# Kernel optimization log

Measured on AMD Instinct MI355X. Metric: run time of the kernel, lower is better.

## Reference

```python
import jax, jax.numpy as jnp
import numpy as np

B, L, DIM, N, D = 8, 273, 1536, 12, 128
ZS, F_HIS = 256, 32  # image tokens per frame, cache_frame_max
EPS = 1e-6


def rmsnorm(x, g, eps=EPS):
    return x * jax.lax.rsqrt(jnp.mean(x * x, axis=-1, keepdims=True) + eps) * g


def rope_apply(x, freqs):
    # x: [B, T, N, D]; freqs: [T, D//2] angles. Rotate consecutive pairs.
    xp = x.reshape(*x.shape[:-1], D // 2, 2)
    c = jnp.cos(freqs)[None, :, None, :]
    s = jnp.sin(freqs)[None, :, None, :]
    o1 = xp[..., 0] * c - xp[..., 1] * s
    o2 = xp[..., 0] * s + xp[..., 1] * c
    return jnp.stack([o1, o2], axis=-1).reshape(x.shape)


def setup_inputs() -> dict:
    key = jax.random.key(0)
    ks = jax.random.split(key, 10)
    rn = lambda k, shp, sc=1.0: jax.random.normal(k, shp, dtype=jnp.float32) * sc
    return {
        "x": rn(ks[0], (B, L, DIM)),
        "w_q": rn(ks[1], (DIM, DIM), 0.02), "b_q": jnp.zeros((DIM,), jnp.float32),
        "w_k": rn(ks[2], (DIM, DIM), 0.02), "b_k": jnp.zeros((DIM,), jnp.float32),
        "w_v": rn(ks[3], (DIM, DIM), 0.02), "b_v": jnp.zeros((DIM,), jnp.float32),
        "w_o": rn(ks[4], (DIM, DIM), 0.02), "b_o": jnp.zeros((DIM,), jnp.float32),
        "g_q": jnp.ones((DIM,), jnp.float32), "g_k": jnp.ones((DIM,), jnp.float32),
        "cache_k": rn(ks[5], (B, F_HIS * L, N, D)),
        "cache_v": rn(ks[6], (B, F_HIS * L, N, D)),
        "rope_table": jax.random.uniform(ks[7], (64, L, D // 2), dtype=jnp.float32) * (2.0 * np.pi),
        "read_rope_indices": jnp.arange(F_HIS, dtype=jnp.int32),
        "current_frame_idx": 20,
    }


def reference(x, w_q, b_q, w_k, b_k, w_v, b_v, w_o, b_o, g_q, g_k,
              cache_k, cache_v, rope_table, read_rope_indices, current_frame_idx):
    b, s = x.shape[:2]
    f = 1  # one new frame per step (s == L)
    # qkv projections with RMSNorm over full dim (pre head split)
    q = rmsnorm(x @ w_q.T + b_q, g_q).reshape(b, s, N, D)
    k = rmsnorm(x @ w_k.T + b_k, g_k).reshape(b, s, N, D)
    v = (x @ w_v.T + b_v).reshape(b, s, N, D)
    # KV-cache ring-buffer store at slot = frame_idx % cache_frame_max
    slot = current_frame_idx % F_HIS
    cache_k = jax.lax.dynamic_update_slice(cache_k, k, (0, slot * L, 0, 0))
    cache_v = jax.lax.dynamic_update_slice(cache_v, v, (0, slot * L, 0, 0))
    # RoPE angles: history for each cache slot, last for the current frame
    freqs_his = rope_table[read_rope_indices].reshape(F_HIS * L, D // 2)
    freqs_last = rope_table[current_frame_idx]  # [L, D//2]
    q_r = rope_apply(q, freqs_last)
    k_r = rope_apply(cache_k, freqs_his)
    # frame-major views: [b, frames, tokens_per_frame, n, d]
    q_r = q_r.reshape(b, f, L, N, D)
    k_r = k_r.reshape(b, F_HIS, L, N, D)
    v_his = cache_v.reshape(b, F_HIS, L, N, D)
    q_img, k_img, v_img = q_r[:, :, :ZS], k_r[:, :, :ZS], v_his[:, :, :ZS]
    # temporal attention per spatial (image) token, non-causal, masked to valid frames
    scale = 1.0 / jnp.sqrt(jnp.asarray(D, jnp.float32))
    scores = jnp.einsum('bfznd,bgznd->bznfg', q_img, k_img) * scale  # [b,zs,n,f,f_his]
    valid = jnp.minimum(current_frame_idx + 1, F_HIS)
    keep = jnp.arange(F_HIS) < valid
    scores = jnp.where(keep[None, None, None, None, :], scores, -1e30)
    p = jax.nn.softmax(scores, axis=-1)
    x_img = jnp.einsum('bznfg,bgznd->bfznd', p, v_img)  # [b, f, zs, n, d]
    # condition tokens bypass attention: pass through v of the current frame
    v_cond = v.reshape(b, f, L, N, D)[:, :, ZS:]
    out = jnp.concatenate([x_img, v_cond], axis=2).reshape(b, s, N * D)
    return out @ w_o.T + b_o


if __name__ == '__main__':
    o = reference(**setup_inputs())
    print(o.shape)
```

## Files before the change

kernel.cpp:

```cpp
#include <hip/hip_runtime.h>
#include <hip/hip_bf16.h>
#include <stdint.h>

typedef unsigned short u16;
typedef __attribute__((ext_vector_type(8))) short bf16x8;
typedef __attribute__((ext_vector_type(4))) float f32x4;

#define B_    8
#define L_    273
#define DIM_  1536
#define NH_   12
#define DH_   128
#define ZS_   256
#define FH_   32
#define MROWS (B_ * L_)
#define MPAD  2304
#define NQKV  4608
#define WN_   (DIM_ * DIM_)
#define WN8_  (WN_ / 8)
#define X8_   (MROWS * DIM_ / 8)
#define XT8_  (MPAD * DIM_ / 8)

#define N0_ 442368
#define N1_ 737280
#define N2_ 1032192
#define N3_ 1327104
#define N4_ 1622016
#define N5_ 1626624
#define N6_ 2167296
#define PREP_BLKS 8466

#define ATTN_ITEMS (B_ * ZS_ * 6)
#define ATTN_BLKS  (ATTN_ITEMS / 2)
#define VCOND_TOT  (B_ * (L_ - ZS_) * DIM_ / 8)
#define VCOND_BLKS ((VCOND_TOT + 255) / 256)

#define KSPLIT 768

#define OFF_XB    0ULL
#define OFF_WB    7077888ULL
#define OFF_WOB   21233664ULL
#define OFF_BQKV  25952256ULL
#define OFF_CQKV  25970688ULL
#define OFF_ATTN  47204352ULL
#define OFF_SC    54282240ULL
#define OFF_RMS   58607616ULL
#define OFF_P0    0ULL
#define OFF_P1    25970688ULL

__device__ __forceinline__ u16 f2bf(float f) {
  __hip_bfloat16 h = __float2bfloat16(f);
  return *reinterpret_cast<u16*>(&h);
}
__device__ __forceinline__ float bf2f(u16 v) {
  uint32_t u = ((uint32_t)v) << 16;
  return __uint_as_float(u);
}

__device__ __forceinline__ void gload_lds16(const u16* g, u16* l) {
  __builtin_amdgcn_global_load_lds(
      (const __attribute__((address_space(1))) void*)g,
      (__attribute__((address_space(3))) void*)l,
      16, 0, 0);
}

__device__ __forceinline__ void cast8(const float* __restrict__ s, u16* __restrict__ d,
                                      int i, int nvalid) {
  uint4 o;
  if (i < nvalid) {
    const float4 a = ((const float4*)s)[i * 2];
    const float4 b = ((const float4*)s)[i * 2 + 1];
    o.x = (uint32_t)f2bf(a.x) | ((uint32_t)f2bf(a.y) << 16);
    o.y = (uint32_t)f2bf(a.z) | ((uint32_t)f2bf(a.w) << 16);
    o.z = (uint32_t)f2bf(b.x) | ((uint32_t)f2bf(b.y) << 16);
    o.w = (uint32_t)f2bf(b.z) | ((uint32_t)f2bf(b.w) << 16);
  } else {
    o = make_uint4(0, 0, 0, 0);
  }
  ((uint4*)d)[i] = o;
}

__global__ __launch_bounds__(256)
void prep_kernel(const float* __restrict__ x, const float* __restrict__ w_q,
                 const float* __restrict__ w_k, const float* __restrict__ w_v,
                 const float* __restrict__ w_o, const float* __restrict__ bq,
                 const float* __restrict__ bk, const float* __restrict__ bv,
                 const float* __restrict__ rope_tb, const int* __restrict__ rope_ix,
                 const int* __restrict__ cf_ptr,
                 u16* __restrict__ xb, u16* __restrict__ wb, u16* __restrict__ wob,
                 float* __restrict__ bqkv, float* __restrict__ sctab) {
  const int t = blockIdx.x * 256 + threadIdx.x;
  if (t < N0_)      cast8(x,   xb,           t,       X8_);
  else if (t < N1_) cast8(w_q, wb,           t - N0_, WN8_);
  else if (t < N2_) cast8(w_k, wb + WN_,     t - N1_, WN8_);
  else if (t < N3_) cast8(w_v, wb + 2 * WN_, t - N2_, WN8_);
  else if (t < N4_) cast8(w_o, wob,          t - N3_, WN8_);
  else if (t < N5_) {
    int i = t - N4_;
    float v;
    if (i < DIM_)          v = bq[i];
    else if (i < 2 * DIM_) v = bk[i - DIM_];
    else                   v = bv[i - 2 * DIM_];
    bqkv[i] = v;
  } else if (t < N6_) {
    int u = t - N5_;
    int j = u & 63;
    int idx = u >> 6;
    int f = idx >> 8, z = idx & 255;
    int fi = (f == 32) ? *cf_ptr : rope_ix[f];
    float fr = rope_tb[((size_t)fi * L_ + z) * 64 + j];
    float sn, cn;
    __sincosf(fr, &sn, &cn);
    *(float2*)&sctab[((size_t)idx << 7) + 2 * j] = make_float2(sn, cn);
  }
}

__global__ __launch_bounds__(256)
void gemm_bt_kernel(const u16* __restrict__ A, const u16* __restrict__ Bm,
                    const float* __restrict__ bias, void* __restrict__ Cv,
                    void* __restrict__ Cv2,
                    int K, int ldc, int Mvalid, int mode, int ksplit) {
  const int nwg = gridDim.x * gridDim.y;
  const int lin = blockIdx.y * gridDim.x + blockIdx.x;
  const int nl = (lin & 7) * (nwg >> 3) + (lin >> 3);
  const int tn = nl % gridDim.x, tm = nl / gridDim.x;

  const int tid = threadIdx.x;
  const int lane = tid & 63;
  const int wid = tid >> 6;
  const int wm = wid >> 1, wn = wid & 1;

  __shared__ __align__(16) u16 As[2][128 * 32];
  __shared__ __align__(16) u16 Bs[2][128 * 32];

  f32x4 acc[4][4] = {};

  const int srow = tid >> 2;
  const int scol = (tid & 3) * 8;
  const u16* Abase = A + (size_t)(tm * 128 + srow) * K + scol;
  const u16* Bbase = Bm + (size_t)(tn * 128 + srow) * K + scol;
  const size_t rstep = (size_t)64 * K;
  const int lofs = srow * 32 + scol;

  const int ko = (lane >> 4) * 8;
  const int rA = wm * 64 + (lane & 15);
  const int rB = wn * 64 + (lane & 15);

  const int k0 = blockIdx.z * ksplit;
  const int k1 = k0 + ksplit;

  gload_lds16(Abase + k0,         &As[0][lofs]);
  gload_lds16(Abase + k0 + rstep, &As[0][64 * 32 + lofs]);
  gload_lds16(Bbase + k0,         &Bs[0][lofs]);
  gload_lds16(Bbase + k0 + rstep, &Bs[0][64 * 32 + lofs]);
  __syncthreads();

  int cur = 0;
  for (int kt = k0; kt < k1; kt += 32) {
    const int nx = cur ^ 1;
    if (kt + 32 < k1) {
      gload_lds16(Abase + kt + 32,         &As[nx][lofs]);
      gload_lds16(Abase + kt + 32 + rstep, &As[nx][64 * 32 + lofs]);
      gload_lds16(Bbase + kt + 32,         &Bs[nx][lofs]);
      gload_lds16(Bbase + kt + 32 + rstep, &Bs[nx][64 * 32 + lofs]);
    }
    bf16x8 af[4], bfr[4];
#pragma unroll
    for (int f = 0; f < 4; ++f) {
      af[f]  = *(const bf16x8*)&As[cur][(rA + f * 16) * 32 + ko];
      bfr[f] = *(const bf16x8*)&Bs[cur][(rB + f * 16) * 32 + ko];
    }
#pragma unroll
    for (int fm = 0; fm < 4; ++fm)
#pragma unroll
      for (int fn = 0; fn < 4; ++fn)
        acc[fm][fn] = __builtin_amdgcn_mfma_f32_16x16x32_bf16(af[fm], bfr[fn], acc[fm][fn], 0, 0, 0);
    __syncthreads();
    cur = nx;
  }

  const int m0 = tm * 128 + wm * 64 + (lane >> 4) * 4;
  const int n0 = tn * 128 + wn * 64 + (lane & 15);
  float* Cf = (mode == 2 && blockIdx.z) ? (float*)Cv2 : (float*)Cv;
#pragma unroll
  for (int fm = 0; fm < 4; ++fm) {
#pragma unroll
    for (int fn = 0; fn < 4; ++fn) {
      const int n = n0 + fn * 16;
      const float bv = (mode == 2) ? 0.f : bias[n];
#pragma unroll
      for (int r = 0; r < 4; ++r) {
        const int m = m0 + fm * 16 + r;
        if (m < Mvalid) {
          const float val = acc[fm][fn][r] + bv;
          if (mode == 1) ((u16*)Cv)[(size_t)m * ldc + n] = f2bf(val);
          else           Cf[(size_t)m * ldc + n] = val;
        }
      }
    }
  }
}

__global__ __launch_bounds__(256)
void rms_kernel(const u16* __restrict__ Cq, float* __restrict__ rms) {
  const int w = blockIdx.x * 4 + (threadIdx.x >> 6);
  const int lane = threadIdx.x & 63;
  const int sec = w & 1;
  const int rid = w >> 1;
  const int b = rid >> 8, z = rid & 255;
  const u16* p = Cq + (size_t)(b * L_ + z) * NQKV + sec * DIM_;
  float ss = 0.f;
#pragma unroll
  for (int j = 0; j < 3; ++j) {
    bf16x8 v = *(const bf16x8*)&p[lane * 8 + j * 512];
#pragma unroll
    for (int e = 0; e < 8; ++e) {
      float f = bf2f((u16)v[e]);
      ss += f * f;
    }
  }
#pragma unroll
  for (int o = 32; o; o >>= 1) ss += __shfl_xor(ss, o);
  if (lane == 0)
    rms[sec * 2048 + rid] = rsqrtf(ss * (1.f / DIM_) + 1e-6f);
}

__global__ __launch_bounds__(256)
void attention_kernel(const u16* __restrict__ Cq, const float* __restrict__ cache_k,
                      const float* __restrict__ cache_v, const float* __restrict__ sctab,
                      const float* __restrict__ rms, const float* __restrict__ g_q,
                      const float* __restrict__ g_k,
                      const int* __restrict__ cf_ptr, u16* __restrict__ attn_in) {
  if (blockIdx.x >= ATTN_BLKS) {
    int i = (blockIdx.x - ATTN_BLKS) * 256 + threadIdx.x;
    if (i < VCOND_TOT) {
      int e = i * 8;
      int col = e % DIM_;
      int r = e / DIM_;
      int b = r / (L_ - ZS_);
      int lz = r % (L_ - ZS_);
      size_t mrow = (size_t)b * L_ + ZS_ + lz;
      *(uint4*)&attn_in[mrow * DIM_ + col] = *(const uint4*)&Cq[mrow * NQKV + 2 * DIM_ + col];
    }
    return;
  }

  __shared__ float sm[2][64][6];
  const int p = threadIdx.x >> 7;
  const int wi = (threadIdx.x >> 6) & 1;
  const int lane = threadIdx.x & 63;
  const int item = blockIdx.x * 2 + p;
  const int hp = item % 6;
  const int z = (item / 6) % ZS_;
  const int b = item / (6 * ZS_);
  const int h = lane >> 5, il = lane & 31;
  const int n = hp * 2 + h;
  const int d0 = il * 4;
  const int cf = *cf_ptr;
  const int slot = cf % FH_;
  const int valid = min(cf + 1, FH_);
  const int g0 = (valid + 1) >> 1;
  const int gs = wi ? g0 : 0;
  const int ge = wi ? valid : g0;

  const size_t crow = (size_t)(b * L_ + z) * NQKV + n * DH_ + d0;
  const float rq = rms[b * ZS_ + z];
  float q0, q1, q2, q3;
  {
    ushort4 qv = *(const ushort4*)&Cq[crow];
    const float4 gq = *(const float4*)&g_q[n * DH_ + d0];
    const float u0 = bf2f(qv.x) * rq * gq.x;
    const float u1 = bf2f(qv.y) * rq * gq.y;
    const float u2 = bf2f(qv.z) * rq * gq.z;
    const float u3 = bf2f(qv.w) * rq * gq.w;
    const float4 scq = *(const float4*)&sctab[((size_t)(32 * ZS_ + z) << 7) + d0];
    q0 = u0 * scq.y - u1 * scq.x;
    q1 = u0 * scq.x + u1 * scq.y;
    q2 = u2 * scq.w - u3 * scq.z;
    q3 = u2 * scq.z + u3 * scq.w;
  }

  float mx = -1e30f, lsum = 0.f;
  float a0 = 0.f, a1 = 0.f, a2 = 0.f, a3 = 0.f;
  for (int g = gs; g < ge; ++g) {
    const float4 sc = *(const float4*)&sctab[((size_t)(g * ZS_ + z) << 7) + d0];
    float k0, k1, k2, k3, v0, v1, v2, v3;
    if (g == slot) {
      ushort4 kv = *(const ushort4*)&Cq[crow + DIM_];
      ushort4 vv = *(const ushort4*)&Cq[crow + 2 * DIM_];
      const float rk = rms[2048 + b * ZS_ + z];
      const float4 gk = *(const float4*)&g_k[n * DH_ + d0];
      k0 = bf2f(kv.x) * rk * gk.x;
      k1 = bf2f(kv.y) * rk * gk.y;
      k2 = bf2f(kv.z) * rk * gk.z;
      k3 = bf2f(kv.w) * rk * gk.w;
      v0 = bf2f(vv.x); v1 = bf2f(vv.y); v2 = bf2f(vv.z); v3 = bf2f(vv.w);
    } else {
      const size_t coff = ((((size_t)b * FH_ + g) * L_ + z) * NH_ + n) * DH_ + d0;
      const float4 kk = *(const float4*)&cache_k[coff];
      const float4 vv = *(const float4*)&cache_v[coff];
      k0 = kk.x; k1 = kk.y; k2 = kk.z; k3 = kk.w;
      v0 = vv.x; v1 = vv.y; v2 = vv.z; v3 = vv.w;
    }
    const float kr0 = k0 * sc.y - k1 * sc.x;
    const float kr1 = k0 * sc.x + k1 * sc.y;
    const float kr2 = k2 * sc.w - k3 * sc.z;
    const float kr3 = k2 * sc.z + k3 * sc.w;
    float part = q0 * kr0 + q1 * kr1 + q2 * kr2 + q3 * kr3;
#pragma unroll
    for (int o = 16; o; o >>= 1) part += __shfl_xor(part, o);
    const float score = part * 0.088388347648318447f;
    const float nm = fmaxf(mx, score);
    const float scl = __expf(mx - nm);
    const float pw = __expf(score - nm);
    lsum = lsum * scl + pw;
    a0 = a0 * scl + pw * v0;
    a1 = a1 * scl + pw * v1;
    a2 = a2 * scl + pw * v2;
    a3 = a3 * scl + pw * v3;
    mx = nm;
  }

  if (wi == 1) {
    sm[p][lane][0] = mx;  sm[p][lane][1] = lsum;
    sm[p][lane][2] = a0;  sm[p][lane][3] = a1;
    sm[p][lane][4] = a2;  sm[p][lane][5] = a3;
  }
  __syncthreads();
  if (wi == 0) {
    const float mB = sm[p][lane][0], lB = sm[p][lane][1];
    const float M = fmaxf(mx, mB);
    const float wA = __expf(mx - M), wB = __expf(mB - M);
    const float L = lsum * wA + lB * wB;
    const float inv = 1.f / L;
    const float o0 = (a0 * wA + sm[p][lane][2] * wB) * inv;
    const float o1 = (a1 * wA + sm[p][lane][3] * wB) * inv;
    const float o2 = (a2 * wA + sm[p][lane][4] * wB) * inv;
    const float o3 = (a3 * wA + sm[p][lane][5] * wB) * inv;
    uint2 o;
    o.x = (uint32_t)f2bf(o0) | ((uint32_t)f2bf(o1) << 16);
    o.y = (uint32_t)f2bf(o2) | ((uint32_t)f2bf(o3) << 16);
    *(uint2*)&attn_in[(size_t)(b * L_ + z) * DIM_ + n * DH_ + d0] = o;
  }
}

__global__ __launch_bounds__(256)
void reduce_kernel(const float* __restrict__ p0, const float* __restrict__ p1,
                   const float* __restrict__ b_o, float* __restrict__ out) {
  const int i = blockIdx.x * 256 + threadIdx.x;
  if (i >= MROWS * DIM_ / 4) return;
  const int col4 = i % (DIM_ / 4);
  const float4 a = ((const float4*)p0)[i];
  const float4 b = ((const float4*)p1)[i];
  const float4 c = ((const float4*)b_o)[col4];
  float4 o;
  o.x = a.x + b.x + c.x;
  o.y = a.y + b.y + c.y;
  o.z = a.z + b.z + c.z;
  o.w = a.w + b.w + c.w;
  ((float4*)out)[i] = o;
}

extern "C" void kernel_launch(void* const* d_in, const int* in_sizes, int n_in,
                              void* d_out, int out_size, void* d_ws, size_t ws_size,
                              hipStream_t stream) {
  const float* x       = (const float*)d_in[0];
  const float* w_q     = (const float*)d_in[1];
  const float* b_q     = (const float*)d_in[2];
  const float* w_k     = (const float*)d_in[3];
  const float* b_k     = (const float*)d_in[4];
  const float* w_v     = (const float*)d_in[5];
  const float* b_v     = (const float*)d_in[6];
  const float* w_o     = (const float*)d_in[7];
  const float* b_o     = (const float*)d_in[8];
  const float* g_q     = (const float*)d_in[9];
  const float* g_k     = (const float*)d_in[10];
  const float* cache_k = (const float*)d_in[11];
  const float* cache_v = (const float*)d_in[12];
  const float* rope_tb = (const float*)d_in[13];
  const int*   rope_ix = (const int*)d_in[14];
  const int*   cf      = (const int*)d_in[15];

  char* ws = (char*)d_ws;
  u16*   xb      = (u16*)(ws + OFF_XB);
  u16*   wb      = (u16*)(ws + OFF_WB);
  u16*   wob     = (u16*)(ws + OFF_WOB);
  float* bqkv    = (float*)(ws + OFF_BQKV);
  u16*   Cq      = (u16*)(ws + OFF_CQKV);
  u16*   attn_in = (u16*)(ws + OFF_ATTN);
  float* sctab   = (float*)(ws + OFF_SC);
  float* rms     = (float*)(ws + OFF_RMS);
  float* p0      = (float*)(ws + OFF_P0);
  float* p1      = (float*)(ws + OFF_P1);

  prep_kernel<<<PREP_BLKS, 256, 0, stream>>>(x, w_q, w_k, w_v, w_o, b_q, b_k, b_v,
                                             rope_tb, rope_ix, cf, xb, wb, wob, bqkv, sctab);

  gemm_bt_kernel<<<dim3(NQKV / 128, MPAD / 128, 1), 256, 0, stream>>>(
      xb, wb, bqkv, Cq, nullptr, DIM_, NQKV, MPAD, 1, DIM_);

  rms_kernel<<<1024, 256, 0, stream>>>(Cq, rms);

  attention_kernel<<<ATTN_BLKS + VCOND_BLKS, 256, 0, stream>>>(
      Cq, cache_k, cache_v, sctab, rms, g_q, g_k, cf, attn_in);

  gemm_bt_kernel<<<dim3(DIM_ / 128, MPAD / 128, 2), 256, 0, stream>>>(
      attn_in, wob, nullptr, p0, p1, DIM_, DIM_, MPAD, 2, KSPLIT);

  reduce_kernel<<<(MROWS * DIM_ / 4 + 255) / 256, 256, 0, stream>>>(p0, p1, b_o, (float*)d_out);
}
```

Before: 221.9 us.

## Widen GEMM K-tile to 64 with XOR-swizzled LDS and explicit vmcnt pipelining

New measurement: 235.6 us. 6.2% more time.

```diff
diff --git a/kernel.cpp b/kernel.cpp
--- a/kernel.cpp
+++ b/kernel.cpp
@@ -130,54 +130,70 @@
   const int wid = tid >> 6;
   const int wm = wid >> 1, wn = wid & 1;
 
-  __shared__ __align__(16) u16 As[2][128 * 32];
-  __shared__ __align__(16) u16 Bs[2][128 * 32];
+  __shared__ __align__(16) u16 As[2][128 * 64];
+  __shared__ __align__(16) u16 Bs[2][128 * 64];
 
   f32x4 acc[4][4] = {};
 
-  const int srow = tid >> 2;
-  const int scol = (tid & 3) * 8;
-  const u16* Abase = A + (size_t)(tm * 128 + srow) * K + scol;
-  const u16* Bbase = Bm + (size_t)(tn * 128 + srow) * K + scol;
-  const size_t rstep = (size_t)64 * K;
-  const int lofs = srow * 32 + scol;
-
-  const int ko = (lane >> 4) * 8;
+  const int sr = tid >> 3;
+  const int cb = (tid & 7) * 16;
+  const int cse = (cb ^ ((sr & 7) << 4)) >> 1;
+  const int k0 = blockIdx.z * ksplit;
+  const u16* Ag = A + (size_t)(tm * 128 + sr) * K + k0 + cse;
+  const u16* Bg = Bm + (size_t)(tn * 128 + sr) * K + k0 + cse;
+  const size_t rstep32 = (size_t)32 * K;
+  const int ldst = sr * 64 + (cb >> 1);
+
+  const int nt = ksplit / 64;
+
+#define STAGE(buf, koff)                                              \
+  {                                                                   \
+    _Pragma("unroll")                                                 \
+    for (int i = 0; i < 4; ++i) {                                     \
+      gload_lds16(Ag + (koff) + i * rstep32, &As[buf][ldst + i * 2048]); \
+      gload_lds16(Bg + (koff) + i * rstep32, &Bs[buf][ldst + i * 2048]); \
+    }                                                                 \
+  }
+
   const int rA = wm * 64 + (lane & 15);
   const int rB = wn * 64 + (lane & 15);
-
-  const int k0 = blockIdx.z * ksplit;
-  const int k1 = k0 + ksplit;
-
-  gload_lds16(Abase + k0,         &As[0][lofs]);
-  gload_lds16(Abase + k0 + rstep, &As[0][64 * 32 + lofs]);
-  gload_lds16(Bbase + k0,         &Bs[0][lofs]);
-  gload_lds16(Bbase + k0 + rstep, &Bs[0][64 * 32 + lofs]);
-  __syncthreads();
+  const int rswz = (lane & 7) << 4;
+  const int c0 = ((lane >> 4) * 16) ^ rswz;
+  const int c1 = (64 + (lane >> 4) * 16) ^ rswz;
+
+  STAGE(0, 0);
 
   int cur = 0;
-  for (int kt = k0; kt < k1; kt += 32) {
-    const int nx = cur ^ 1;
-    if (kt + 32 < k1) {
-      gload_lds16(Abase + kt + 32,         &As[nx][lofs]);
-      gload_lds16(Abase + kt + 32 + rstep, &As[nx][64 * 32 + lofs]);
-      gload_lds16(Bbase + kt + 32,         &Bs[nx][lofs]);
-      gload_lds16(Bbase + kt + 32 + rstep, &Bs[nx][64 * 32 + lofs]);
-    }
-    bf16x8 af[4], bfr[4];
+  for (int t = 0; t < nt; ++t) {
+    __builtin_amdgcn_s_barrier();
+    asm volatile("" ::: "memory");
+    if (t + 1 < nt) {
+      STAGE(cur ^ 1, (t + 1) * 64);
+      asm volatile("s_waitcnt vmcnt(8)" ::: "memory");
+    } else {
+      asm volatile("s_waitcnt vmcnt(0)" ::: "memory");
+    }
+    __builtin_amdgcn_s_barrier();
+    asm volatile("" ::: "memory");
+
+    bf16x8 af[2][4], bfr[2][4];
 #pragma unroll
     for (int f = 0; f < 4; ++f) {
-      af[f]  = *(const bf16x8*)&As[cur][(rA + f * 16) * 32 + ko];
-      bfr[f] = *(const bf16x8*)&Bs[cur][(rB + f * 16) * 32 + ko];
-    }
-#pragma unroll
-    for (int fm = 0; fm < 4; ++fm)
-#pragma unroll
-      for (int fn = 0; fn < 4; ++fn)
-        acc[fm][fn] = __builtin_amdgcn_mfma_f32_16x16x32_bf16(af[fm], bfr[fn], acc[fm][fn], 0, 0, 0);
-    __syncthreads();
-    cur = nx;
-  }
+      af[0][f]  = *(const bf16x8*)&As[cur][(rA + f * 16) * 64 + (c0 >> 1)];
+      af[1][f]  = *(const bf16x8*)&As[cur][(rA + f * 16) * 64 + (c1 >> 1)];
+      bfr[0][f] = *(const bf16x8*)&Bs[cur][(rB + f * 16) * 64 + (c0 >> 1)];
+      bfr[1][f] = *(const bf16x8*)&Bs[cur][(rB + f * 16) * 64 + (c1 >> 1)];
+    }
+#pragma unroll
+    for (int ks = 0; ks < 2; ++ks)
+#pragma unroll
+      for (int fm = 0; fm < 4; ++fm)
+#pragma unroll
+        for (int fn = 0; fn < 4; ++fn)
+          acc[fm][fn] = __builtin_amdgcn_mfma_f32_16x16x32_bf16(af[ks][fm], bfr[ks][fn], acc[fm][fn], 0, 0, 0);
+    cur ^= 1;
+  }
+#undef STAGE
 
   const int m0 = tm * 128 + wm * 64 + (lane >> 4) * 4;
   const int n0 = tn * 128 + wn * 64 + (lane & 15);
```
